# Optimization experiments

Hardware: AMD Instinct MI355X
Metric: run time of the kernel (lower is better)

## Reference

```python
import jax, jax.numpy as jnp
import numpy as np

N = 2048        # nodes
IN_DIM = 128    # input feature dim
K = 8           # channels
D = 32          # per-channel dim (C_dim)
ITERS = 4       # routing iterations
BETA = 1.0      # attention temperature
EPS = 1e-12     # F.normalize eps


def l2norm(x):
    # F.normalize(x, dim=-1): x / max(||x||_2, eps)
    n = jnp.linalg.norm(x, axis=-1, keepdims=True)
    return x / jnp.maximum(n, EPS)


def setup_inputs() -> dict:
    key = jax.random.key(0)
    k1, k2, k3, k4 = jax.random.split(key, 4)
    adj = jax.random.randint(k1, (N, N), 0, 2, dtype=jnp.int32)
    features = jax.random.normal(k2, (N, IN_DIM), dtype=jnp.float32)
    # parameters initialized ~ N(0,1) as in init_parameters
    W = jax.random.normal(k3, (K, IN_DIM, D), dtype=jnp.float32)
    b = jax.random.normal(k4, (K, D), dtype=jnp.float32)
    return {"adj": adj, "features": features, "W": W, "b": b}


def reference(adj, features, W, b):
    mask = (adj > 0)[None, :, :]                         # [1, N, N]
    # per-channel projection + row L2 normalize -> Z: [K, N, D]
    Z = l2norm(jnp.einsum('nd,kdc->knc', features, W) + b[:, None, :])
    for _ in range(ITERS):
        # per-channel masked attention scores [K, N, N]
        att = jnp.einsum('knc,kmc->knm', Z, Z)
        att = jnp.where(mask, att, 0.0) / BETA
        # softmax across channels (dim=2 in torch after cat == K axis here)
        att = jax.nn.softmax(att, axis=0)
        att = jnp.where(mask, att, 0.0)
        # weighted aggregate + residual + L2 normalize
        Z = l2norm(Z + jnp.einsum('knm,kmc->knc', att, Z))
    # concat channels along feature dim -> [N, K*D]
    return jnp.transpose(Z, (1, 0, 2)).reshape(N, K * D)
```

## Files before the change

kernel.cpp:

```cpp
#include <hip/hip_runtime.h>
#include <hip/hip_bf16.h>
#include <hip/hip_fp16.h>

#define NN 2048
#define KK 8
#define DD 32
#define ZSZ (KK * NN * DD)

#define TW(row, slot) (((row) << 4) + ((((slot) ^ (((row) >> 1) & 3))) << 2))
#define TW2(row, wo) (((row) << 4) + (((((wo) >> 2) ^ (((row) >> 1) & 3))) << 2) + ((wo) & 3))

typedef __attribute__((ext_vector_type(8))) short short8;
typedef __attribute__((ext_vector_type(4))) short short4v;
typedef __attribute__((ext_vector_type(4))) float f32x4;
typedef __attribute__((ext_vector_type(4))) unsigned int u32x4;

union UU { u32x4 q; short8 v; unsigned int u[4]; };
union U2 { uint2 q; short4v v; unsigned int u[2]; };

__device__ __forceinline__ unsigned int bfr(float x) {
  unsigned int u = __float_as_uint(x);
  return (u + 0x7fffu + ((u >> 16) & 1u)) >> 16;
}
__device__ __forceinline__ float bf2f(unsigned int h) {
  return __uint_as_float(h << 16);
}
__device__ __forceinline__ unsigned int packp(float a, float b) {
  union { __hip_bfloat162 h; unsigned int u; } cv;
  cv.h = __float22bfloat162_rn(make_float2(a, b));
  return cv.u;
}
__device__ __forceinline__ f32x4 MF(short8 a, short8 b, f32x4 c) {
  return __builtin_amdgcn_mfma_f32_16x16x32_bf16(a, b, c, 0, 0, 0);
}
__device__ __forceinline__ f32x4 MF16(short4v a, short4v b, f32x4 c) {
  return __builtin_amdgcn_mfma_f32_16x16x16bf16_1k(a, b, c, 0, 0, 0);
}
__device__ __forceinline__ short8 as_s8(u32x4 x) { UU u; u.q = x; return u.v; }

__global__ __launch_bounds__(256) void pm_kernel(const float* __restrict__ feat,
                                                 const float* __restrict__ W,
                                                 const float* __restrict__ bias,
                                                 unsigned short* __restrict__ Zghi,
                                                 unsigned short* __restrict__ Zthi,
                                                 const int* __restrict__ adj,
                                                 unsigned int* __restrict__ mbits) {
  __shared__ float fsh[1024];
  const int t = threadIdx.x;
  if (blockIdx.x < 256) {
    const int nb = blockIdx.x * 8;
    const int k = t >> 5, c = t & 31;
    *(float4*)&fsh[4 * t] = *(const float4*)&feat[nb * 128 + 4 * t];
    float s[8];
#pragma unroll
    for (int j = 0; j < 8; ++j) s[j] = bias[k * DD + c];
    const float* w = W + (k * 128) * DD + c;
    __syncthreads();
#pragma unroll 4
    for (int d = 0; d < 128; ++d) {
      float wv = w[d * DD];
#pragma unroll
      for (int j = 0; j < 8; ++j) s[j] = fmaf(fsh[j * 128 + d], wv, s[j]);
    }
    unsigned int hi[8];
#pragma unroll
    for (int j = 0; j < 8; ++j) {
      float sq = s[j] * s[j];
#pragma unroll
      for (int off = 16; off > 0; off >>= 1) sq += __shfl_xor(sq, off, 32);
      float z = s[j] / fmaxf(sqrtf(sq), 1e-12f);
      hi[j] = bfr(z);
      Zghi[(k * NN + nb + j) * DD + c] = (unsigned short)hi[j];
    }
    uint4 tp = make_uint4(hi[0] | (hi[1] << 16), hi[2] | (hi[3] << 16),
                          hi[4] | (hi[5] << 16), hi[6] | (hi[7] << 16));
    *(uint4*)&Zthi[(size_t)k * DD * NN + (size_t)c * NN + nb] = tp;
  } else {
    const int base = (blockIdx.x - 256) * 1024 + t;
    const int lane = t & 63;
    int v[4];
#pragma unroll
    for (int rr = 0; rr < 4; ++rr) v[rr] = adj[base + 256 * rr];
#pragma unroll
    for (int rr = 0; rr < 4; ++rr) {
      int idx = base + 256 * rr;
      unsigned long long b = __ballot(v[rr] > 0);
      if (lane == 0) mbits[idx >> 5] = (unsigned int)b;
      if (lane == 32) mbits[idx >> 5] = (unsigned int)(b >> 32);
    }
  }
}

template <int NCt>
__global__ __launch_bounds__(256) void rp_kernel(const __half* __restrict__ part,
                                                 unsigned short* __restrict__ Zghi,
                                                 unsigned short* __restrict__ Zthi) {
  __shared__ unsigned short T[DD][33];
  const int t = threadIdx.x;
  const int k = blockIdx.x >> 6, mt = blockIdx.x & 63;
  const int m0 = mt * 32;
  const int mloc = t >> 3, c4 = t & 7;
  const size_t idx = (size_t)(k * NN + m0 + mloc) * DD + 4 * c4;
  uint2 zb = *(const uint2*)&Zghi[idx];
  float4 v;
  v.x = bf2f(zb.x & 0xffffu);
  v.y = __uint_as_float(zb.x & 0xffff0000u);
  v.z = bf2f(zb.y & 0xffffu);
  v.w = __uint_as_float(zb.y & 0xffff0000u);
#pragma unroll
  for (int j = 0; j < NCt; ++j) {
    const __half2* ph = (const __half2*)&part[(size_t)j * ZSZ + idx];
    float2 a = __half22float2(ph[0]);
    float2 b = __half22float2(ph[1]);
    v.x += a.x; v.y += a.y; v.z += b.x; v.w += b.y;
  }
  float sq = v.x * v.x + v.y * v.y + v.z * v.z + v.w * v.w;
  sq += __shfl_xor(sq, 1, 8);
  sq += __shfl_xor(sq, 2, 8);
  sq += __shfl_xor(sq, 4, 8);
  const float sc = 1.0f / fmaxf(sqrtf(sq), 1e-12f);
  float z[4] = {v.x * sc, v.y * sc, v.z * sc, v.w * sc};
  unsigned int hi[4];
#pragma unroll
  for (int e = 0; e < 4; ++e) {
    hi[e] = bfr(z[e]);
    T[4 * c4 + e][mloc] = (unsigned short)hi[e];
  }
  *(uint2*)&Zghi[idx] = make_uint2(hi[0] | (hi[1] << 16), hi[2] | (hi[3] << 16));
  __syncthreads();
  const int cloc = t >> 3, m4 = t & 7;
  unsigned int o0 = (unsigned int)T[cloc][4 * m4 + 0] | ((unsigned int)T[cloc][4 * m4 + 1] << 16);
  unsigned int o1 = (unsigned int)T[cloc][4 * m4 + 2] | ((unsigned int)T[cloc][4 * m4 + 3] << 16);
  *(uint2*)&Zthi[(size_t)k * DD * NN + (size_t)cloc * NN + m0 + 4 * m4] = make_uint2(o0, o1);
}

template <int NS>
__global__ __launch_bounds__(256, 2) void iter_kernel(const unsigned short* __restrict__ Zghi,
                                                      const unsigned short* __restrict__ Zthi,
                                                      const unsigned int* __restrict__ mbits,
                                                      __half* __restrict__ part) {
  __shared__ __align__(16) unsigned int lds[20480];
  const int t = threadIdx.x;
  const int w = t >> 6;
  const int lane = t & 63;
  const int l15 = lane & 15;
  const int g = lane >> 4;
  const int nw = blockIdx.x * 64 + w * 16;
  const int mchunk = blockIdx.y * (NS * 32);

  const unsigned int* Zg = (const unsigned int*)Zghi;
  const unsigned int* Zt = (const unsigned int*)Zthi;

  short8 A[KK];
#pragma unroll
  for (int k = 0; k < KK; ++k)
    A[k] = as_s8(*(const u32x4*)&Zg[(size_t)(k * NN + nw + l15) * 16 + 4 * g]);

  unsigned int mword[NS];
#pragma unroll
  for (int q4 = 0; q4 < NS / 4; ++q4) {
    uint4 m4 = *(const uint4*)&mbits[(size_t)(nw + l15) * 64 + (mchunk >> 5) + 4 * q4];
    mword[4 * q4 + 0] = m4.x; mword[4 * q4 + 1] = m4.y;
    mword[4 * q4 + 2] = m4.z; mword[4 * q4 + 3] = m4.w;
  }

  f32x4 O[KK][2];
#pragma unroll
  for (int k = 0; k < KK; ++k)
#pragma unroll
    for (int ch = 0; ch < 2; ++ch) O[k][ch] = {0.0f, 0.0f, 0.0f, 0.0f};

  const int sqd = t & 3;
  const int sr0 = t >> 2;

  u32x4 Lgh[4], Lth[4];
  auto dl_g = [&](int mb) {
#pragma unroll
    for (int j = 0; j < 4; ++j) {
      int r = 64 * j + sr0;
      int k = r >> 5, rm = r & 31;
      Lgh[j] = *(const u32x4*)&Zg[(size_t)(k * NN + mb + rm) * 16 + 4 * sqd];
    }
  };
  auto wr_g = [&](int buf) {
#pragma unroll
    for (int j = 0; j < 4; ++j)
      *(u32x4*)&lds[buf * 4096 + TW(64 * j + sr0, sqd)] = Lgh[j];
  };
  auto dl_t = [&](int mb) {
#pragma unroll
    for (int j = 0; j < 4; ++j) {
      int r = 64 * j + sr0;
      int k = r >> 5, rm = r & 31;
      Lth[j] = *(const u32x4*)&Zt[(size_t)k * (NN * 16) + (size_t)rm * (NN / 2) + (mb >> 1) + 4 * sqd];
    }
  };
  auto wr_t = [&](int buf) {
#pragma unroll
    for (int j = 0; j < 4; ++j)
      *(u32x4*)&lds[12288 + buf * 4096 + TW(64 * j + sr0, sqd)] = Lth[j];
  };

  auto gram = [&](int gbuf, int sub, f32x4* S) {
#pragma unroll
    for (int k = 0; k < KK; ++k) {
      u32x4 bh = *(const u32x4*)&lds[gbuf * 4096 + TW(k * 32 + 16 * sub + l15, g)];
      f32x4 z = {0.0f, 0.0f, 0.0f, 0.0f};
      S[k] = MF(as_s8(bh), A[k], z);
    }
  };
  auto finish = [&](f32x4* S, int tbuf, int sub, unsigned int mw) {
#pragma unroll
    for (int r = 0; r < 4; ++r) {
      float e[KK];
      float sum = 0.0f;
#pragma unroll
      for (int k = 0; k < KK; ++k) { e[k] = __expf(S[k][r]); sum += e[k]; }
      float f = ((mw >> (16 * sub + 4 * g + r)) & 1u) ? __builtin_amdgcn_rcpf(sum) : 0.0f;
#pragma unroll
      for (int k = 0; k < KK; ++k) S[k][r] = e[k] * f;
    }
#pragma unroll
    for (int k = 0; k < KK; ++k) {
      U2 pa;
      pa.u[0] = packp(S[k][0], S[k][1]);
      pa.u[1] = packp(S[k][2], S[k][3]);
#pragma unroll
      for (int ch = 0; ch < 2; ++ch) {
        int row = k * 32 + 16 * ch + l15;
        U2 bv;
        bv.q = *(const uint2*)&lds[12288 + tbuf * 4096 + TW2(row, 8 * sub + 2 * g)];
        O[k][ch] = MF16(pa.v, bv.v, O[k][ch]);
      }
    }
  };

  dl_g(mchunk); wr_g(0);
  if (NS > 1) { dl_g(mchunk + 32); wr_g(1); }
  dl_t(mchunk); wr_t(0);
  if (NS > 2) dl_g(mchunk + 64);
  if (NS > 1) dl_t(mchunk + 32);
  __syncthreads();

  f32x4 Scur[KK], Snxt[KK];
  gram(0, 0, Scur);

#pragma unroll
  for (int st = 0; st < NS; ++st) {
    if (st + 2 < NS) wr_g((st + 2) % 3);
    if (st + 1 < NS) wr_t((st + 1) & 1);
    if (st + 3 < NS) dl_g(mchunk + (st + 3) * 32);
    if (st + 2 < NS) dl_t(mchunk + (st + 2) * 32);
    const unsigned int mw = mword[st];

    gram(st % 3, 1, Snxt);
    finish(Scur, st & 1, 0, mw);
    if (st + 1 < NS) gram((st + 1) % 3, 0, Scur);
    finish(Snxt, st & 1, 1, mw);
    __syncthreads();
  }

  __half* dst = part + (size_t)blockIdx.y * ZSZ;
#pragma unroll
  for (int k = 0; k < KK; ++k)
#pragma unroll
    for (int ch = 0; ch < 2; ++ch) {
      f32x4 o = O[k][ch];
#pragma unroll
      for (int r = 0; r < 4; ++r)
        dst[(size_t)(k * NN + nw + 4 * g + r) * DD + 16 * ch + l15] = __float2half_rn(o[r]);
    }
}

template <int NCt>
__global__ __launch_bounds__(256) void ro_kernel(const unsigned short* __restrict__ Zghi,
                                                 const __half* __restrict__ part,
                                                 float* __restrict__ out) {
  const int n = blockIdx.x, t = threadIdx.x;
  const int k = t >> 5, c = t & 31;
  const size_t idx = (size_t)(k * NN + n) * DD + c;
  float v = bf2f((unsigned int)Zghi[idx]);
#pragma unroll
  for (int j = 0; j < NCt; ++j) v += __half2float(part[(size_t)j * ZSZ + idx]);
  float sq = v * v;
#pragma unroll
  for (int off = 16; off > 0; off >>= 1) sq += __shfl_xor(sq, off, 32);
  out[n * (KK * DD) + t] = v / fmaxf(sqrtf(sq), 1e-12f);
}

extern "C" void kernel_launch(void* const* d_in, const int* in_sizes, int n_in,
                              void* d_out, int out_size, void* d_ws, size_t ws_size,
                              hipStream_t stream) {
  const int* adj = (const int*)d_in[0];
  const float* feat = (const float*)d_in[1];
  const float* W = (const float*)d_in[2];
  const float* b = (const float*)d_in[3];
  float* out = (float*)d_out;

  int NC = 16;
  while (NC > 4) {
    size_t need = (size_t)ZSZ * 2 * 2 + (size_t)NN * 64 * 4 + (size_t)NC * ZSZ * 2;
    if (need <= ws_size) break;
    NC >>= 1;
  }

  unsigned short* Zghi = (unsigned short*)d_ws;
  unsigned short* Zthi = Zghi + ZSZ;
  unsigned int* mbits = (unsigned int*)(Zthi + ZSZ);
  __half* part = (__half*)(mbits + NN * 64);

  pm_kernel<<<256 + 4096, 256, 0, stream>>>(feat, W, b, Zghi, Zthi, adj, mbits);

  for (int it = 0; it < 4; ++it) {
    if (NC == 16)
      iter_kernel<4><<<dim3(32, 16), 256, 0, stream>>>(Zghi, Zthi, mbits, part);
    else if (NC == 8)
      iter_kernel<8><<<dim3(32, 8), 256, 0, stream>>>(Zghi, Zthi, mbits, part);
    else
      iter_kernel<16><<<dim3(32, 4), 256, 0, stream>>>(Zghi, Zthi, mbits, part);
    if (it < 3) {
      if (NC == 16)
        rp_kernel<16><<<512, 256, 0, stream>>>(part, Zghi, Zthi);
      else if (NC == 8)
        rp_kernel<8><<<512, 256, 0, stream>>>(part, Zghi, Zthi);
      else
        rp_kernel<4><<<512, 256, 0, stream>>>(part, Zghi, Zthi);
    } else {
      if (NC == 16)
        ro_kernel<16><<<NN, 256, 0, stream>>>(Zghi, part, out);
      else if (NC == 8)
        ro_kernel<8><<<NN, 256, 0, stream>>>(Zghi, part, out);
      else
        ro_kernel<4><<<NN, 256, 0, stream>>>(Zghi, part, out);
    }
  }
}
```

Baseline: 180.4 us.

## Fuse all stages into one cooperative persistent kernel with grid syncs

```diff
diff --git a/kernel.cpp b/kernel.cpp
--- a/kernel.cpp
+++ b/kernel.cpp
@@ -1,6 +1,9 @@
 #include <hip/hip_runtime.h>
 #include <hip/hip_bf16.h>
 #include <hip/hip_fp16.h>
+#include <hip/hip_cooperative_groups.h>
+
+namespace cg = cooperative_groups;
 
 #define NN 2048
 #define KK 8
@@ -37,6 +40,257 @@
   return __builtin_amdgcn_mfma_f32_16x16x16bf16_1k(a, b, c, 0, 0, 0);
 }
 __device__ __forceinline__ short8 as_s8(u32x4 x) { UU u; u.q = x; return u.v; }
+
+__global__ __launch_bounds__(256, 2) void mega_kernel(
+    const float* feat, const float* W, const float* bias, const int* adj,
+    unsigned short* Zghi, unsigned short* Zthi, unsigned int* mbits,
+    __half* part, float* out) {
+  __shared__ __align__(16) unsigned int lds[20480];
+  cg::grid_group grid = cg::this_grid();
+  const int bx = blockIdx.x;
+  const int t = threadIdx.x;
+  const int w = t >> 6;
+  const int lane = t & 63;
+  const int l15 = lane & 15;
+  const int g = lane >> 4;
+
+  unsigned int* Zg = (unsigned int*)Zghi;
+  unsigned int* Zt = (unsigned int*)Zthi;
+
+  {
+    const int nb = bx * 4;
+    const int k = t >> 5, c = t & 31;
+    float* fsh = (float*)lds;
+    if (t < 128) *(float4*)&fsh[4 * t] = *(const float4*)&feat[nb * 128 + 4 * t];
+    float s[4];
+#pragma unroll
+    for (int j = 0; j < 4; ++j) s[j] = bias[k * DD + c];
+    __syncthreads();
+    const float* wp = W + (k * 128) * DD + c;
+#pragma unroll 4
+    for (int d = 0; d < 128; ++d) {
+      float wv = wp[d * DD];
+#pragma unroll
+      for (int j = 0; j < 4; ++j) s[j] = fmaf(fsh[j * 128 + d], wv, s[j]);
+    }
+    unsigned int hi[4];
+#pragma unroll
+    for (int j = 0; j < 4; ++j) {
+      float sq = s[j] * s[j];
+#pragma unroll
+      for (int off = 16; off > 0; off >>= 1) sq += __shfl_xor(sq, off, 32);
+      float z = s[j] / fmaxf(sqrtf(sq), 1e-12f);
+      hi[j] = bfr(z);
+      Zghi[(k * NN + nb + j) * DD + c] = (unsigned short)hi[j];
+    }
+    *(uint2*)&Zthi[(size_t)k * DD * NN + (size_t)c * NN + nb] =
+        make_uint2(hi[0] | (hi[1] << 16), hi[2] | (hi[3] << 16));
+
+    const int base = bx * 8192 + t;
+#pragma unroll
+    for (int q = 0; q < 4; ++q) {
+      int v[8];
+#pragma unroll
+      for (int r = 0; r < 8; ++r) v[r] = adj[base + 256 * (8 * q + r)];
+#pragma unroll
+      for (int r = 0; r < 8; ++r) {
+        int idx = base + 256 * (8 * q + r);
+        unsigned long long b = __ballot(v[r] > 0);
+        if (lane == 0) mbits[idx >> 5] = (unsigned int)b;
+        if (lane == 32) mbits[idx >> 5] = (unsigned int)(b >> 32);
+      }
+    }
+  }
+  grid.sync();
+
+  const int nblk = bx & 31;
+  const int chunk = bx >> 5;
+  const int nw = nblk * 64 + w * 16;
+  const int mchunk = chunk * 128;
+  const int sqd = t & 3;
+  const int sr0 = t >> 2;
+
+#pragma unroll 1
+  for (int it = 0; it < 4; ++it) {
+    {
+      short8 A[KK];
+#pragma unroll
+      for (int k = 0; k < KK; ++k)
+        A[k] = as_s8(*(const u32x4*)&Zg[(size_t)(k * NN + nw + l15) * 16 + 4 * g]);
+
+      unsigned int mword[4];
+      {
+        uint4 m4 = *(const uint4*)&mbits[(size_t)(nw + l15) * 64 + (mchunk >> 5)];
+        mword[0] = m4.x; mword[1] = m4.y; mword[2] = m4.z; mword[3] = m4.w;
+      }
+
+      f32x4 O[KK][2];
+#pragma unroll
+      for (int k = 0; k < KK; ++k)
+#pragma unroll
+        for (int ch = 0; ch < 2; ++ch) O[k][ch] = {0.0f, 0.0f, 0.0f, 0.0f};
+
+      u32x4 Lgh[4], Lth[4];
+      auto dl_g = [&](int mb) {
+#pragma unroll
+        for (int j = 0; j < 4; ++j) {
+          int r = 64 * j + sr0;
+          int k = r >> 5, rm = r & 31;
+          Lgh[j] = *(const u32x4*)&Zg[(size_t)(k * NN + mb + rm) * 16 + 4 * sqd];
+        }
+      };
+      auto wr_g = [&](int buf) {
+#pragma unroll
+        for (int j = 0; j < 4; ++j)
+          *(u32x4*)&lds[buf * 4096 + TW(64 * j + sr0, sqd)] = Lgh[j];
+      };
+      auto dl_t = [&](int mb) {
+#pragma unroll
+        for (int j = 0; j < 4; ++j) {
+          int r = 64 * j + sr0;
+          int k = r >> 5, rm = r & 31;
+          Lth[j] = *(const u32x4*)&Zt[(size_t)k * (NN * 16) + (size_t)rm * (NN / 2) + (mb >> 1) + 4 * sqd];
+        }
+      };
+      auto wr_t = [&](int buf) {
+#pragma unroll
+        for (int j = 0; j < 4; ++j)
+          *(u32x4*)&lds[12288 + buf * 4096 + TW(64 * j + sr0, sqd)] = Lth[j];
+      };
+      auto gram = [&](int gbuf, int sub, f32x4* S) {
+#pragma unroll
+        for (int k = 0; k < KK; ++k) {
+          u32x4 bh = *(const u32x4*)&lds[gbuf * 4096 + TW(k * 32 + 16 * sub + l15, g)];
+          f32x4 z = {0.0f, 0.0f, 0.0f, 0.0f};
+          S[k] = MF(as_s8(bh), A[k], z);
+        }
+      };
+      auto finish = [&](f32x4* S, int tbuf, int sub, unsigned int mw) {
+#pragma unroll
+        for (int r = 0; r < 4; ++r) {
+          float e[KK];
+          float sum = 0.0f;
+#pragma unroll
+          for (int k = 0; k < KK; ++k) { e[k] = __expf(S[k][r]); sum += e[k]; }
+          float f = ((mw >> (16 * sub + 4 * g + r)) & 1u) ? __builtin_amdgcn_rcpf(sum) : 0.0f;
+#pragma unroll
+          for (int k = 0; k < KK; ++k) S[k][r] = e[k] * f;
+        }
+#pragma unroll
+        for (int k = 0; k < KK; ++k) {
+          U2 pa;
+          pa.u[0] = packp(S[k][0], S[k][1]);
+          pa.u[1] = packp(S[k][2], S[k][3]);
+#pragma unroll
+          for (int ch = 0; ch < 2; ++ch) {
+            int row = k * 32 + 16 * ch + l15;
+            U2 bv;
+            bv.q = *(const uint2*)&lds[12288 + tbuf * 4096 + TW2(row, 8 * sub + 2 * g)];
+            O[k][ch] = MF16(pa.v, bv.v, O[k][ch]);
+          }
+        }
+      };
+
+      dl_g(mchunk); wr_g(0);
+      dl_g(mchunk + 32); wr_g(1);
+      dl_t(mchunk); wr_t(0);
+      dl_g(mchunk + 64);
+      dl_t(mchunk + 32);
+      __syncthreads();
+
+      f32x4 Scur[KK], Snxt[KK];
+      gram(0, 0, Scur);
+
+#pragma unroll
+      for (int st = 0; st < 4; ++st) {
+        if (st + 2 < 4) wr_g((st + 2) % 3);
+        if (st + 1 < 4) wr_t((st + 1) & 1);
+        if (st + 3 < 4) dl_g(mchunk + (st + 3) * 32);
+        if (st + 2 < 4) dl_t(mchunk + (st + 2) * 32);
+        const unsigned int mw = mword[st];
+
+        gram(st % 3, 1, Snxt);
+        finish(Scur, st & 1, 0, mw);
+        if (st + 1 < 4) gram((st + 1) % 3, 0, Scur);
+        finish(Snxt, st & 1, 1, mw);
+        __syncthreads();
+      }
+
+      __half* dst = part + (size_t)chunk * ZSZ;
+#pragma unroll
+      for (int k = 0; k < KK; ++k)
+#pragma unroll
+        for (int ch = 0; ch < 2; ++ch) {
+          f32x4 o = O[k][ch];
+#pragma unroll
+          for (int r = 0; r < 4; ++r)
+            dst[(size_t)(k * NN + nw + 4 * g + r) * DD + 16 * ch + l15] = __float2half_rn(o[r]);
+        }
+    }
+    grid.sync();
+
+    if (it < 3) {
+      {
+        unsigned short* T = (unsigned short*)lds;
+        const int k = bx >> 6, mt = bx & 63;
+        const int m0 = mt * 32;
+        const int mloc = t >> 3, c4 = t & 7;
+        const size_t idx = (size_t)(k * NN + m0 + mloc) * DD + 4 * c4;
+        uint2 zb = *(const uint2*)&Zghi[idx];
+        float4 v;
+        v.x = bf2f(zb.x & 0xffffu);
+        v.y = __uint_as_float(zb.x & 0xffff0000u);
+        v.z = bf2f(zb.y & 0xffffu);
+        v.w = __uint_as_float(zb.y & 0xffff0000u);
+#pragma unroll
+        for (int j = 0; j < 16; ++j) {
+          const __half2* ph = (const __half2*)&part[(size_t)j * ZSZ + idx];
+          float2 a = __half22float2(ph[0]);
+          float2 bb = __half22float2(ph[1]);
+          v.x += a.x; v.y += a.y; v.z += bb.x; v.w += bb.y;
+        }
+        float sq = v.x * v.x + v.y * v.y + v.z * v.z + v.w * v.w;
+        sq += __shfl_xor(sq, 1, 8);
+        sq += __shfl_xor(sq, 2, 8);
+        sq += __shfl_xor(sq, 4, 8);
+        const float sc = 1.0f / fmaxf(sqrtf(sq), 1e-12f);
+        float z[4] = {v.x * sc, v.y * sc, v.z * sc, v.w * sc};
+        unsigned int hi[4];
+#pragma unroll
+        for (int e = 0; e < 4; ++e) {
+          hi[e] = bfr(z[e]);
+          T[(4 * c4 + e) * 33 + mloc] = (unsigned short)hi[e];
+        }
+        *(uint2*)&Zghi[idx] = make_uint2(hi[0] | (hi[1] << 16), hi[2] | (hi[3] << 16));
+        __syncthreads();
+        const int cloc = t >> 3, m4i = t & 7;
+        unsigned int o0 = (unsigned int)T[cloc * 33 + 4 * m4i + 0] |
+                          ((unsigned int)T[cloc * 33 + 4 * m4i + 1] << 16);
+        unsigned int o1 = (unsigned int)T[cloc * 33 + 4 * m4i + 2] |
+                          ((unsigned int)T[cloc * 33 + 4 * m4i + 3] << 16);
+        *(uint2*)&Zthi[(size_t)k * DD * NN + (size_t)cloc * NN + m0 + 4 * m4i] =
+            make_uint2(o0, o1);
+      }
+      grid.sync();
+    }
+  }
+
+  {
+    const int k = t >> 5, c = t & 31;
+#pragma unroll
+    for (int jj = 0; jj < 4; ++jj) {
+      const int n = bx * 4 + jj;
+      const size_t idx = (size_t)(k * NN + n) * DD + c;
+      float v = bf2f((unsigned int)Zghi[idx]);
+#pragma unroll
+      for (int j = 0; j < 16; ++j) v += __half2float(part[(size_t)j * ZSZ + idx]);
+      float sq = v * v;
+#pragma unroll
+      for (int off = 16; off > 0; off >>= 1) sq += __shfl_xor(sq, off, 32);
+      out[n * (KK * DD) + t] = v / fmaxf(sqrtf(sq), 1e-12f);
+    }
+  }
+}
 
 __global__ __launch_bounds__(256) void pm_kernel(const float* __restrict__ feat,
                                                  const float* __restrict__ W,
@@ -91,7 +345,6 @@
   }
 }
 
-template <int NCt>
 __global__ __launch_bounds__(256) void rp_kernel(const __half* __restrict__ part,
                                                  unsigned short* __restrict__ Zghi,
                                                  unsigned short* __restrict__ Zthi) {
@@ -108,7 +361,7 @@
   v.z = bf2f(zb.y & 0xffffu);
   v.w = __uint_as_float(zb.y & 0xffff0000u);
 #pragma unroll
-  for (int j = 0; j < NCt; ++j) {
+  for (int j = 0; j < 16; ++j) {
     const __half2* ph = (const __half2*)&part[(size_t)j * ZSZ + idx];
     float2 a = __half22float2(ph[0]);
     float2 b = __half22float2(ph[1]);
@@ -134,7 +387,6 @@
   *(uint2*)&Zthi[(size_t)k * DD * NN + (size_t)cloc * NN + m0 + 4 * m4] = make_uint2(o0, o1);
 }
 
-template <int NS>
 __global__ __launch_bounds__(256, 2) void iter_kernel(const unsigned short* __restrict__ Zghi,
                                                       const unsigned short* __restrict__ Zthi,
                                                       const unsigned int* __restrict__ mbits,
@@ -146,7 +398,7 @@
   const int l15 = lane & 15;
   const int g = lane >> 4;
   const int nw = blockIdx.x * 64 + w * 16;
-  const int mchunk = blockIdx.y * (NS * 32);
+  const int mchunk = blockIdx.y * 128;
 
   const unsigned int* Zg = (const unsigned int*)Zghi;
   const unsigned int* Zt = (const unsigned int*)Zthi;
@@ -156,12 +408,10 @@
   for (int k = 0; k < KK; ++k)
     A[k] = as_s8(*(const u32x4*)&Zg[(size_t)(k * NN + nw + l15) * 16 + 4 * g]);
 
-  unsigned int mword[NS];
-#pragma unroll
-  for (int q4 = 0; q4 < NS / 4; ++q4) {
-    uint4 m4 = *(const uint4*)&mbits[(size_t)(nw + l15) * 64 + (mchunk >> 5) + 4 * q4];
-    mword[4 * q4 + 0] = m4.x; mword[4 * q4 + 1] = m4.y;
-    mword[4 * q4 + 2] = m4.z; mword[4 * q4 + 3] = m4.w;
+  unsigned int mword[4];
+  {
+    uint4 m4 = *(const uint4*)&mbits[(size_t)(nw + l15) * 64 + (mchunk >> 5)];
+    mword[0] = m4.x; mword[1] = m4.y; mword[2] = m4.z; mword[3] = m4.w;
   }
 
   f32x4 O[KK][2];
@@ -200,7 +450,6 @@
     for (int j = 0; j < 4; ++j)
       *(u32x4*)&lds[12288 + buf * 4096 + TW(64 * j + sr0, sqd)] = Lth[j];
   };
-
   auto gram = [&](int gbuf, int sub, f32x4* S) {
 #pragma unroll
     for (int k = 0; k < KK; ++k) {
@@ -236,26 +485,26 @@
   };
 
   dl_g(mchunk); wr_g(0);
-  if (NS > 1) { dl_g(mchunk + 32); wr_g(1); }
+  dl_g(mchunk + 32); wr_g(1);
   dl_t(mchunk); wr_t(0);
-  if (NS > 2) dl_g(mchunk + 64);
-  if (NS > 1) dl_t(mchunk + 32);
+  dl_g(mchunk + 64);
+  dl_t(mchunk + 32);
   __syncthreads();
 
   f32x4 Scur[KK], Snxt[KK];
   gram(0, 0, Scur);
 
 #pragma unroll
-  for (int st = 0; st < NS; ++st) {
-    if (st + 2 < NS) wr_g((st + 2) % 3);
-    if (st + 1 < NS) wr_t((st + 1) & 1);
-    if (st + 3 < NS) dl_g(mchunk + (st + 3) * 32);
-    if (st + 2 < NS) dl_t(mchunk + (st + 2) * 32);
+  for (int st = 0; st < 4; ++st) {
+    if (st + 2 < 4) wr_g((st + 2) % 3);
+    if (st + 1 < 4) wr_t((st + 1) & 1);
+    if (st + 3 < 4) dl_g(mchunk + (st + 3) * 32);
+    if (st + 2 < 4) dl_t(mchunk + (st + 2) * 32);
     const unsigned int mw = mword[st];
 
     gram(st % 3, 1, Snxt);
     finish(Scur, st & 1, 0, mw);
-    if (st + 1 < NS) gram((st + 1) % 3, 0, Scur);
+    if (st + 1 < 4) gram((st + 1) % 3, 0, Scur);
     finish(Snxt, st & 1, 1, mw);
     __syncthreads();
   }
@@ -272,7 +521,6 @@
     }
 }
 
-template <int NCt>
 __global__ __launch_bounds__(256) void ro_kernel(const unsigned short* __restrict__ Zghi,
                                                  const __half* __restrict__ part,
                                                  float* __restrict__ out) {
@@ -281,7 +529,7 @@
   const size_t idx = (size_t)(k * NN + n) * DD + c;
   float v = bf2f((unsigned int)Zghi[idx]);
 #pragma unroll
-  for (int j = 0; j < NCt; ++j) v += __half2float(part[(size_t)j * ZSZ + idx]);
+  for (int j = 0; j < 16; ++j) v += __half2float(part[(size_t)j * ZSZ + idx]);
   float sq = v * v;
 #pragma unroll
   for (int off = 16; off > 0; off >>= 1) sq += __shfl_xor(sq, off, 32);
@@ -297,41 +545,29 @@
   const float* b = (const float*)d_in[3];
   float* out = (float*)d_out;
 
-  int NC = 16;
-  while (NC > 4) {
-    size_t need = (size_t)ZSZ * 2 * 2 + (size_t)NN * 64 * 4 + (size_t)NC * ZSZ * 2;
-    if (need <= ws_size) break;
-    NC >>= 1;
-  }
-
   unsigned short* Zghi = (unsigned short*)d_ws;
   unsigned short* Zthi = Zghi + ZSZ;
   unsigned int* mbits = (unsigned int*)(Zthi + ZSZ);
   __half* part = (__half*)(mbits + NN * 64);
 
+  bool coop_ok = false;
+  int maxb = 0;
+  if (hipOccupancyMaxActiveBlocksPerMultiprocessor(&maxb, mega_kernel, 256, 0) == hipSuccess &&
+      maxb >= 2) {
+    void* kargs[] = {(void*)&feat, (void*)&W, (void*)&b, (void*)&adj,
+                     (void*)&Zghi, (void*)&Zthi, (void*)&mbits, (void*)&part, (void*)&out};
+    if (hipLaunchCooperativeKernel((const void*)mega_kernel, dim3(512), dim3(256), kargs, 0,
+                                   stream) == hipSuccess)
+      coop_ok = true;
+  }
+  if (coop_ok) return;
+
   pm_kernel<<<256 + 4096, 256, 0, stream>>>(feat, W, b, Zghi, Zthi, adj, mbits);
-
   for (int it = 0; it < 4; ++it) {
-    if (NC == 16)
-      iter_kernel<4><<<dim3(32, 16), 256, 0, stream>>>(Zghi, Zthi, mbits, part);
-    else if (NC == 8)
-      iter_kernel<8><<<dim3(32, 8), 256, 0, stream>>>(Zghi, Zthi, mbits, part);
+    iter_kernel<<<dim3(32, 16), 256, 0, stream>>>(Zghi, Zthi, mbits, part);
+    if (it < 3)
+      rp_kernel<<<512, 256, 0, stream>>>(part, Zghi, Zthi);
     else
-      iter_kernel<16><<<dim3(32, 4), 256, 0, stream>>>(Zghi, Zthi, mbits, part);
-    if (it < 3) {
-      if (NC == 16)
-        rp_kernel<16><<<512, 256, 0, stream>>>(part, Zghi, Zthi);
-      else if (NC == 8)
-        rp_kernel<8><<<512, 256, 0, stream>>>(part, Zghi, Zthi);
-      else
-        rp_kernel<4><<<512, 256, 0, stream>>>(part, Zghi, Zthi);
-    } else {
-      if (NC == 16)
-        ro_kernel<16><<<NN, 256, 0, stream>>>(Zghi, part, out);
-      else if (NC == 8)
-        ro_kernel<8><<<NN, 256, 0, stream>>>(Zghi, part, out);
-      else
-        ro_kernel<4><<<NN, 256, 0, stream>>>(Zghi, part, out);
-    }
-  }
-}
+      ro_kernel<<<NN, 256, 0, stream>>>(Zghi, part, out);
+  }
+}
```

Result: no change. 180.0 us (median of 2 runs) (-0.2%).
